# Kernel tuning notes

Hardware: AMD Instinct MI355X
Metric: run time of the kernel (lower is better)

The kernel has to match this reference:

```python
import jax, jax.numpy as jnp
import numpy as np

N_CENTROIDS = 1024
NSAMPLES = 32
RADIUS = 0.5
BN_EPS = 1e-5


def fps(xyz, npoint):
    """Iterative farthest point sampling. xyz: [B,N,3] -> idx [B,npoint] int32."""
    B, N, _ = xyz.shape

    def step(carry, _):
        dist_min, farthest = carry  # [B,N], [B]
        centroid = jnp.take_along_axis(xyz, farthest[:, None, None], axis=1)  # [B,1,3]
        d = jnp.sum((xyz - centroid) ** 2, axis=-1)  # [B,N]
        dist_min = jnp.minimum(dist_min, d)
        nxt = jnp.argmax(dist_min, axis=1).astype(jnp.int32)
        return (dist_min, nxt), farthest

    init = (jnp.full((B, N), 1e10, xyz.dtype), jnp.zeros((B,), jnp.int32))
    _, idx = jax.lax.scan(step, init, None, length=npoint)
    return idx.T  # [B, npoint]


def gather_points(p, idx):
    """p: [B,N,C], idx: [B,...] int -> [B,...,C]."""
    return jax.vmap(lambda pp, ii: pp[ii])(p, idx)


def square_distance(a, b):
    """a: [B,S,3], b: [B,N,3] -> [B,S,N] squared distances (GEMM form)."""
    aa = jnp.sum(a * a, axis=-1)[:, :, None]
    bb = jnp.sum(b * b, axis=-1)[:, None, :]
    ab = jnp.einsum('bsc,bnc->bsn', a, b)
    return aa + bb - 2.0 * ab


def ball_query(centroids, xyz, nsample, radius):
    B, S, _ = centroids.shape
    N = xyz.shape[1]
    sqrdists = square_distance(centroids, xyz)  # [B,S,N]
    base = jnp.broadcast_to(jnp.arange(N, dtype=jnp.int32), (B, S, N))
    group_idx = jnp.where(sqrdists > radius * radius, N, base)
    group_idx = jnp.sort(group_idx, axis=-1)[:, :, :nsample]  # [B,S,K]
    first = group_idx[:, :, :1]
    group_idx = jnp.where(group_idx == N, first, group_idx)
    return group_idx


def batchnorm2d(h, gamma, beta):
    """Training-mode BN over (B,H,W) per channel. h: [B,C,H,W]."""
    mean = jnp.mean(h, axis=(0, 2, 3), keepdims=True)
    var = jnp.mean((h - mean) ** 2, axis=(0, 2, 3), keepdims=True)
    hhat = (h - mean) * jax.lax.rsqrt(var + BN_EPS)
    return gamma[None, :, None, None] * hhat + beta[None, :, None, None]


def conv1x1(h, w, b):
    """h: [B,C,H,W], w: [O,C] -> [B,O,H,W]."""
    return jnp.einsum('bchw,oc->bohw', h, w) + b[None, :, None, None]


def setup_inputs() -> dict:
    key = jax.random.key(0)
    ks = jax.random.split(key, 4)
    B, N, D = 16, 4096, 3
    mlp0, mlp1, in_ch = 64, 128, 6
    return {
        'x': jax.random.normal(ks[0], (B, N, 3), jnp.float32),
        'points': jax.random.normal(ks[1], (B, N, D), jnp.float32),
        'w1': jax.random.normal(ks[2], (mlp0, in_ch), jnp.float32) * 0.1,
        'b1': jnp.zeros((mlp0,), jnp.float32),
        'gamma1': jnp.ones((mlp0,), jnp.float32),
        'beta1': jnp.zeros((mlp0,), jnp.float32),
        'w2': jax.random.normal(ks[3], (mlp1, mlp0), jnp.float32) * 0.1,
        'b2': jnp.zeros((mlp1,), jnp.float32),
        'gamma2': jnp.ones((mlp1,), jnp.float32),
        'beta2': jnp.zeros((mlp1,), jnp.float32),
    }


def reference(x, points, w1, b1, gamma1, beta1, w2, b2, gamma2, beta2):
    # FPS -> centroids
    cidx = fps(x, N_CENTROIDS)                      # [B,S]
    centroids = gather_points(x, cidx)              # [B,S,3]
    # Ball-query grouping
    idx = ball_query(centroids, x, NSAMPLES, RADIUS)  # [B,S,K]
    grouped_xyz = gather_points(x, idx) - centroids[:, :, None, :]  # [B,S,K,3]
    grouped_pts = jnp.concatenate([grouped_xyz, gather_points(points, idx)], axis=-1)  # [B,S,K,C]
    # g_points.transpose(1,3): [B,S,K,C] -> [B,C,K,S]
    h = jnp.transpose(grouped_pts, (0, 3, 2, 1))
    h = jax.nn.relu(batchnorm2d(conv1x1(h, w1, b1), gamma1, beta1))
    h = jax.nn.relu(batchnorm2d(conv1x1(h, w2, b2), gamma2, beta2))
    out = jnp.max(h, axis=2)            # [B,mlp1,S]
    out = jnp.transpose(out, (0, 2, 1))  # [B,S,mlp1]
    return centroids, out
```

## Files before the change

kernel.cpp:

```cpp
#include <hip/hip_runtime.h>
#include <stdint.h>
#include <math.h>

constexpr int BB = 16;
constexpr int NN = 4096;
constexpr int SS = 1024;
constexpr int KK = 32;
constexpr int C3 = 128;
constexpr float R2 = 0.25f;
constexpr int STAT_BLOCKS = 2048;

__device__ __forceinline__ float sumsq3(float x, float y, float z) {
#pragma clang fp contract(off)
  return (x * x + y * y) + z * z;
}

__device__ __forceinline__ float ball_d(float aa, float bb, float cx, float cy,
                                        float cz, float px, float py, float pz) {
#pragma clang fp contract(off)
  float ab = (cx * px + cy * py) + cz * pz;
  return (aa + bb) - 2.0f * ab;
}

__device__ __forceinline__ unsigned long long u64max(unsigned long long a,
                                                     unsigned long long b) {
  return a > b ? a : b;
}

#define DPP_KEY_STEP(CTRL, k)                                                  \
  {                                                                            \
    int lo_ = (int)(unsigned)(k);                                              \
    int hi_ = (int)(unsigned)((k) >> 32);                                      \
    int slo_ = __builtin_amdgcn_update_dpp(0, lo_, (CTRL), 0xf, 0xf, true);    \
    int shi_ = __builtin_amdgcn_update_dpp(0, hi_, (CTRL), 0xf, 0xf, true);    \
    unsigned long long o_ =                                                    \
        ((unsigned long long)(unsigned)shi_ << 32) | (unsigned)(unsigned)slo_; \
    (k) = u64max((k), o_);                                                     \
  }

__global__ void k_bb(const float* __restrict__ x, float* __restrict__ bb) {
  int i = blockIdx.x * blockDim.x + threadIdx.x;
  if (i >= BB * NN) return;
  float x0 = x[3 * i], x1 = x[3 * i + 1], x2 = x[3 * i + 2];
  bb[i] = sumsq3(x0, x1, x2);
}

__global__ __launch_bounds__(256) void k_fps(const float* __restrict__ x,
                                             int* __restrict__ cidx) {
  __shared__ float xs[NN], ys[NN], zs[NN];
  __shared__ unsigned long long wkey[2][4];
  int b = blockIdx.x, t = threadIdx.x;
  const float* xb = x + (size_t)b * NN * 3;
  float px[16], py[16], pz[16], dmin[16];
  unsigned lo_[16];
#pragma unroll
  for (int j = 0; j < 16; ++j) {
    int n = t + j * 256;
    float a0 = xb[3 * n], a1 = xb[3 * n + 1], a2 = xb[3 * n + 2];
    px[j] = a0; py[j] = a1; pz[j] = a2;
    xs[n] = a0; ys[n] = a1; zs[n] = a2;
    dmin[j] = 1e10f;
    lo_[j] = (unsigned)(NN - 1 - n);
  }
  if (t == 0) cidx[b * SS] = 0;
  __syncthreads();
  int far = 0;
  int w = t >> 6;
  for (int it = 1; it < SS; ++it) {
    float cx = xs[far], cy = ys[far], cz = zs[far];
    float best = -1.0f;
    unsigned blo = 0u;
#pragma unroll
    for (int j = 0; j < 16; ++j) {
      float dx = px[j] - cx, dy = py[j] - cy, dz = pz[j] - cz;
      float d = sumsq3(dx, dy, dz);
      float dm = fminf(dmin[j], d);
      dmin[j] = dm;
      if (dm > best) { best = dm; blo = lo_[j]; }
    }
    unsigned long long key =
        ((unsigned long long)__float_as_uint(best) << 32) | blo;
    DPP_KEY_STEP(0xB1, key);
    DPP_KEY_STEP(0x4E, key);
    DPP_KEY_STEP(0x124, key);
    DPP_KEY_STEP(0x128, key);
    {
      int lo2 = __builtin_amdgcn_ds_swizzle((int)(unsigned)key, 0x401F);
      int hi2 = __builtin_amdgcn_ds_swizzle((int)(unsigned)(key >> 32), 0x401F);
      unsigned long long o =
          ((unsigned long long)(unsigned)hi2 << 32) | (unsigned)lo2;
      key = u64max(key, o);
    }
    key = u64max(key, __shfl_xor(key, 32));
    int buf = it & 1;
    if ((t & 63) == 0) wkey[buf][w] = key;
    __syncthreads();
    unsigned long long k0 = wkey[buf][0], k1 = wkey[buf][1];
    unsigned long long k2 = wkey[buf][2], k3 = wkey[buf][3];
    unsigned long long kk = u64max(u64max(k0, k1), u64max(k2, k3));
    far = NN - 1 - (int)(unsigned)(kk & 0xffffffffu);
    if (t == 0) cidx[b * SS + it] = far;
  }
}

__global__ void k_gather(const float* __restrict__ x, const int* __restrict__ cidx,
                         float* __restrict__ outc, float* __restrict__ aa) {
  int i = blockIdx.x * blockDim.x + threadIdx.x;
  if (i >= BB * SS) return;
  int b = i >> 10;
  int n = cidx[i];
  const float* p = x + ((size_t)b * NN + n) * 3;
  float cx = p[0], cy = p[1], cz = p[2];
  outc[3 * i] = cx; outc[3 * i + 1] = cy; outc[3 * i + 2] = cz;
  aa[i] = sumsq3(cx, cy, cz);
}

__global__ __launch_bounds__(256) void k_ball(const float* __restrict__ x,
                                              const float* __restrict__ cent,
                                              const float* __restrict__ aa,
                                              const float* __restrict__ bb,
                                              int* __restrict__ idx) {
  int gw = (blockIdx.x * 256 + threadIdx.x) >> 6;
  int lane = threadIdx.x & 63;
  if (gw >= BB * SS) return;
  int b = gw >> 10;
  const float* xb = x + (size_t)b * NN * 3;
  const float* bbb = bb + b * NN;
  float cx = cent[3 * gw], cy = cent[3 * gw + 1], cz = cent[3 * gw + 2];
  float a = aa[gw];
  int* out = idx + (size_t)gw * KK;
  int found = 0, firstN = 0;
  for (int c0 = 0; c0 < NN && found < KK; c0 += 64) {
    int n = c0 + lane;
    float px = xb[3 * n], py = xb[3 * n + 1], pz = xb[3 * n + 2];
    float d = ball_d(a, bbb[n], cx, cy, cz, px, py, pz);
    bool pred = (d <= R2);
    unsigned long long m = __ballot(pred);
    if (found == 0 && m) firstN = c0 + (__ffsll((unsigned long long)m) - 1);
    if (pred) {
      int pos = found + __popcll(m & ((1ull << lane) - 1ull));
      if (pos < KK) out[pos] = n;
    }
    found += __popcll(m);
  }
  if (lane == 0 && found < KK) {
    for (int k = found; k < KK; ++k) out[k] = firstN;
  }
}

__global__ __launch_bounds__(256) void k_stats1(
    const float* __restrict__ x, const float* __restrict__ pts,
    const float* __restrict__ cent, const int* __restrict__ idx,
    const float* __restrict__ w1, const float* __restrict__ b1,
    float* __restrict__ partial1) {
  __shared__ float feat[KK][6];
  __shared__ float red[4][64][2];
  int t = threadIdx.x;
  int c = t & 63, kq = t >> 6;
  float w[6];
#pragma unroll
  for (int j = 0; j < 6; ++j) w[j] = w1[c * 6 + j];
  float bias = b1[c];
  float sum = 0.f, sq = 0.f;
  for (int gi = 0; gi < 8; ++gi) {
    int g = blockIdx.x * 8 + gi;
    int b = g >> 10;
    if (t < KK) {
      int n = idx[(size_t)g * KK + t];
      const float* p = x + ((size_t)b * NN + n) * 3;
      feat[t][0] = p[0] - cent[3 * g];
      feat[t][1] = p[1] - cent[3 * g + 1];
      feat[t][2] = p[2] - cent[3 * g + 2];
      const float* q = pts + ((size_t)b * NN + n) * 3;
      feat[t][3] = q[0];
      feat[t][4] = q[1];
      feat[t][5] = q[2];
    }
    __syncthreads();
    for (int k = kq * 8; k < kq * 8 + 8; ++k) {
      float a = bias;
#pragma unroll
      for (int j = 0; j < 6; ++j) a += w[j] * feat[k][j];
      sum += a;
      sq += a * a;
    }
    __syncthreads();
  }
  red[kq][c][0] = sum;
  red[kq][c][1] = sq;
  __syncthreads();
  if (t < 64) {
    float s = ((red[0][t][0] + red[1][t][0]) + red[2][t][0]) + red[3][t][0];
    float q = ((red[0][t][1] + red[1][t][1]) + red[2][t][1]) + red[3][t][1];
    partial1[(size_t)(blockIdx.x * 64 + t) * 2] = s;
    partial1[(size_t)(blockIdx.x * 64 + t) * 2 + 1] = q;
  }
}

__global__ void k_red1(const float* __restrict__ partial1,
                       const float* __restrict__ gamma, const float* __restrict__ beta,
                       float* __restrict__ sc1) {
  __shared__ double rd[64][4][2];
  int t = threadIdx.x;
  int c = t & 63, q = t >> 6;
  double s = 0.0, qq = 0.0;
  for (int blk = q * 512; blk < q * 512 + 512; ++blk) {
    s += partial1[(size_t)(blk * 64 + c) * 2];
    qq += partial1[(size_t)(blk * 64 + c) * 2 + 1];
  }
  rd[c][q][0] = s; rd[c][q][1] = qq;
  __syncthreads();
  if (t < 64) {
    double S = ((rd[t][0][0] + rd[t][1][0]) + rd[t][2][0]) + rd[t][3][0];
    double Q = ((rd[t][0][1] + rd[t][1][1]) + rd[t][2][1]) + rd[t][3][1];
    const double cnt = (double)BB * KK * SS;
    double mean = S / cnt;
    double var = Q / cnt - mean * mean;
    float scale = gamma[t] * (float)(1.0 / sqrt(var + 1e-5));
    float shift = beta[t] - (float)mean * scale;
    sc1[t] = scale;
    sc1[64 + t] = shift;
  }
}

__global__ __launch_bounds__(256) void k_stats2(
    const float* __restrict__ x, const float* __restrict__ pts,
    const float* __restrict__ cent, const int* __restrict__ idx,
    const float* __restrict__ w1, const float* __restrict__ b1,
    const float* __restrict__ sc1, const float* __restrict__ w2,
    const float* __restrict__ b2, float* __restrict__ partial2,
    float* __restrict__ gmax, float* __restrict__ gmin) {
  __shared__ float feat[KK][6];
  __shared__ float vT[64][36];
  __shared__ float w2sA[64][68];
  __shared__ float w2sB[64][68];
  __shared__ float red[C3][4][2];
  __shared__ float mx[C3][4], mn[C3][4];
  int t = threadIdx.x;
  int c1 = t & 63, kq = t >> 6;
  int c2p = t >> 2, ks = t & 3;
  {
    int r = t >> 1, h = (t & 1) * 32;
    float* dst = (r < 64 ? &w2sA[r][h] : &w2sB[r - 64][h]);
    const float* src = w2 + r * 64 + h;
    for (int c = 0; c < 32; ++c) dst[c] = src[c];
  }
  float w1r[6];
#pragma unroll
  for (int j = 0; j < 6; ++j) w1r[j] = w1[c1 * 6 + j];
  float bias1 = b1[c1];
  float scale1 = sc1[c1], shift1 = sc1[64 + c1];
  float bias2a = b2[c2p], bias2b = b2[c2p + 64];
  float sumA = 0.f, sqA = 0.f, sumB = 0.f, sqB = 0.f;
  for (int gi = 0; gi < 8; ++gi) {
    int g = blockIdx.x * 8 + gi;
    int b = g >> 10;
    if (t < KK) {
      int n = idx[(size_t)g * KK + t];
      const float* p = x + ((size_t)b * NN + n) * 3;
      feat[t][0] = p[0] - cent[3 * g];
      feat[t][1] = p[1] - cent[3 * g + 1];
      feat[t][2] = p[2] - cent[3 * g + 2];
      const float* q = pts + ((size_t)b * NN + n) * 3;
      feat[t][3] = q[0];
      feat[t][4] = q[1];
      feat[t][5] = q[2];
    }
    __syncthreads();
    for (int k = kq * 8; k < kq * 8 + 8; ++k) {
      float a = bias1;
#pragma unroll
      for (int j = 0; j < 6; ++j) a += w1r[j] * feat[k][j];
      vT[c1][k] = fmaxf(0.f, a * scale1 + shift1);
    }
    __syncthreads();
    float accA[8] = {0, 0, 0, 0, 0, 0, 0, 0};
    float accB[8] = {0, 0, 0, 0, 0, 0, 0, 0};
#pragma unroll
    for (int c0 = 0; c0 < 64; c0 += 4) {
      float4 wa4 = *(const float4*)&w2sA[c2p][c0];
      float4 wb4 = *(const float4*)&w2sB[c2p][c0];
#pragma unroll
      for (int cc = 0; cc < 4; ++cc) {
        int c = c0 + cc;
        float4 v0 = *(const float4*)&vT[c][ks * 8];
        float4 v1 = *(const float4*)&vT[c][ks * 8 + 4];
        float wa = (cc == 0 ? wa4.x : cc == 1 ? wa4.y : cc == 2 ? wa4.z : wa4.w);
        float wb = (cc == 0 ? wb4.x : cc == 1 ? wb4.y : cc == 2 ? wb4.z : wb4.w);
        accA[0] += wa * v0.x; accA[1] += wa * v0.y; accA[2] += wa * v0.z; accA[3] += wa * v0.w;
        accA[4] += wa * v1.x; accA[5] += wa * v1.y; accA[6] += wa * v1.z; accA[7] += wa * v1.w;
        accB[0] += wb * v0.x; accB[1] += wb * v0.y; accB[2] += wb * v0.z; accB[3] += wb * v0.w;
        accB[4] += wb * v1.x; accB[5] += wb * v1.y; accB[6] += wb * v1.z; accB[7] += wb * v1.w;
      }
    }
    float mA = -1e30f, mB = -1e30f, nA = 1e30f, nB = 1e30f;
#pragma unroll
    for (int i = 0; i < 8; ++i) {
      float a = accA[i] + bias2a;
      sumA += a; sqA += a * a;
      mA = fmaxf(mA, a); nA = fminf(nA, a);
      float c_ = accB[i] + bias2b;
      sumB += c_; sqB += c_ * c_;
      mB = fmaxf(mB, c_); nB = fminf(nB, c_);
    }
    mx[c2p][ks] = mA;      mn[c2p][ks] = nA;
    mx[c2p + 64][ks] = mB; mn[c2p + 64][ks] = nB;
    __syncthreads();
    if (t < C3) {
      float M = fmaxf(fmaxf(mx[t][0], mx[t][1]), fmaxf(mx[t][2], mx[t][3]));
      float m_ = fminf(fminf(mn[t][0], mn[t][1]), fminf(mn[t][2], mn[t][3]));
      gmax[(size_t)g * C3 + t] = M;
      gmin[(size_t)g * C3 + t] = m_;
    }
  }
  red[c2p][ks][0] = sumA;      red[c2p][ks][1] = sqA;
  red[c2p + 64][ks][0] = sumB; red[c2p + 64][ks][1] = sqB;
  __syncthreads();
  if (t < C3) {
    float s = ((red[t][0][0] + red[t][1][0]) + red[t][2][0]) + red[t][3][0];
    float q = ((red[t][0][1] + red[t][1][1]) + red[t][2][1]) + red[t][3][1];
    partial2[(size_t)(blockIdx.x * 128 + t) * 2] = s;
    partial2[(size_t)(blockIdx.x * 128 + t) * 2 + 1] = q;
  }
}

__global__ void k_red2(const float* __restrict__ partial2,
                       const float* __restrict__ gamma, const float* __restrict__ beta,
                       float* __restrict__ sc2) {
  __shared__ double rd[128][4][2];
  int t = threadIdx.x;
  int c = t & 127, q = t >> 7;
  double s = 0.0, qq = 0.0;
  for (int blk = q * 512; blk < q * 512 + 512; ++blk) {
    s += partial2[(size_t)(blk * 128 + c) * 2];
    qq += partial2[(size_t)(blk * 128 + c) * 2 + 1];
  }
  rd[c][q][0] = s; rd[c][q][1] = qq;
  __syncthreads();
  if (t < 128) {
    double S = ((rd[t][0][0] + rd[t][1][0]) + rd[t][2][0]) + rd[t][3][0];
    double Q = ((rd[t][0][1] + rd[t][1][1]) + rd[t][2][1]) + rd[t][3][1];
    const double cnt = (double)BB * KK * SS;
    double mean = S / cnt;
    double var = Q / cnt - mean * mean;
    float scale = gamma[t] * (float)(1.0 / sqrt(var + 1e-5));
    float shift = beta[t] - (float)mean * scale;
    sc2[t] = scale;
    sc2[128 + t] = shift;
  }
}

__global__ void k_final2(const float* __restrict__ gmin,
                         const float* __restrict__ sc2, float* __restrict__ outp) {
  int i = blockIdx.x * blockDim.x + threadIdx.x;
  if (i >= BB * SS * C3) return;
  int c = i & (C3 - 1);
  float scale = sc2[c], shift = sc2[C3 + c];
  float a = (scale >= 0.f) ? outp[i] : gmin[i];
  outp[i] = fmaxf(0.f, a * scale + shift);
}

extern "C" void kernel_launch(void* const* d_in, const int* in_sizes, int n_in,
                              void* d_out, int out_size, void* d_ws, size_t ws_size,
                              hipStream_t stream) {
  const float* x      = (const float*)d_in[0];
  const float* pts    = (const float*)d_in[1];
  const float* w1     = (const float*)d_in[2];
  const float* b1     = (const float*)d_in[3];
  const float* gamma1 = (const float*)d_in[4];
  const float* beta1  = (const float*)d_in[5];
  const float* w2     = (const float*)d_in[6];
  const float* b2     = (const float*)d_in[7];
  const float* gamma2 = (const float*)d_in[8];
  const float* beta2  = (const float*)d_in[9];

  float* out_cent = (float*)d_out;
  float* out_feat = (float*)d_out + (size_t)BB * SS * 3;

  char* w = (char*)d_ws;
  int* cidx    = (int*)w;   w += (size_t)BB * SS * 4;
  float* aa    = (float*)w; w += (size_t)BB * SS * 4;
  float* bb    = (float*)w; w += (size_t)BB * NN * 4;
  int* idx     = (int*)w;   w += (size_t)BB * SS * KK * 4;
  float* p1    = (float*)w; w += (size_t)STAT_BLOCKS * 64 * 2 * 4;
  float* p2    = (float*)w; w += (size_t)STAT_BLOCKS * 128 * 2 * 4;
  float* sc1   = (float*)w; w += 64 * 2 * 4;
  float* sc2   = (float*)w; w += 128 * 2 * 4;
  float* gmin  = (float*)w; w += (size_t)BB * SS * C3 * 4;

  k_bb<<<(BB * NN + 255) / 256, 256, 0, stream>>>(x, bb);
  k_fps<<<BB, 256, 0, stream>>>(x, cidx);
  k_gather<<<(BB * SS + 255) / 256, 256, 0, stream>>>(x, cidx, out_cent, aa);
  k_ball<<<(BB * SS) / 4, 256, 0, stream>>>(x, out_cent, aa, bb, idx);
  k_stats1<<<STAT_BLOCKS, 256, 0, stream>>>(x, pts, out_cent, idx, w1, b1, p1);
  k_red1<<<1, 256, 0, stream>>>(p1, gamma1, beta1, sc1);
  k_stats2<<<STAT_BLOCKS, 256, 0, stream>>>(x, pts, out_cent, idx, w1, b1, sc1,
                                            w2, b2, p2, out_feat, gmin);
  k_red2<<<1, 512, 0, stream>>>(p2, gamma2, beta2, sc2);
  k_final2<<<(BB * SS * C3 + 255) / 256, 256, 0, stream>>>(gmin, sc2, out_feat);
}
```

Measured before the change: 964.1 us.

## Streamline FPS reduction with float max, ballot, and broadcast centroid coordinates

```diff
diff --git a/kernel.cpp b/kernel.cpp
--- a/kernel.cpp
+++ b/kernel.cpp
@@ -27,16 +27,23 @@
   return a > b ? a : b;
 }
 
-#define DPP_KEY_STEP(CTRL, k)                                                  \
+#define DPP_MAXF(CTRL, v)                                                      \
   {                                                                            \
-    int lo_ = (int)(unsigned)(k);                                              \
-    int hi_ = (int)(unsigned)((k) >> 32);                                      \
-    int slo_ = __builtin_amdgcn_update_dpp(0, lo_, (CTRL), 0xf, 0xf, true);    \
-    int shi_ = __builtin_amdgcn_update_dpp(0, hi_, (CTRL), 0xf, 0xf, true);    \
-    unsigned long long o_ =                                                    \
-        ((unsigned long long)(unsigned)shi_ << 32) | (unsigned)(unsigned)slo_; \
-    (k) = u64max((k), o_);                                                     \
-  }
+    int s_ = __builtin_amdgcn_update_dpp(0, __float_as_int(v), (CTRL), 0xf,    \
+                                         0xf, true);                           \
+    (v) = fmaxf((v), __int_as_float(s_));                                      \
+  }
+
+__device__ __forceinline__ float xor32maxf(float v) {
+#if __has_builtin(__builtin_amdgcn_permlane32_swap)
+  typedef int v2i __attribute__((ext_vector_type(2)));
+  v2i r = __builtin_amdgcn_permlane32_swap(__float_as_int(v), __float_as_int(v),
+                                           false, false);
+  return fmaxf(fmaxf(v, __int_as_float(r[0])), __int_as_float(r[1]));
+#else
+  return fmaxf(v, __shfl_xor(v, 32));
+#endif
+}
 
 __global__ void k_bb(const float* __restrict__ x, float* __restrict__ bb) {
   int i = blockIdx.x * blockDim.x + threadIdx.x;
@@ -47,60 +54,68 @@
 
 __global__ __launch_bounds__(256) void k_fps(const float* __restrict__ x,
                                              int* __restrict__ cidx) {
-  __shared__ float xs[NN], ys[NN], zs[NN];
   __shared__ unsigned long long wkey[2][4];
+  __shared__ float4 wxyz[2][4];
+  __shared__ int farhist[SS];
   int b = blockIdx.x, t = threadIdx.x;
   const float* xb = x + (size_t)b * NN * 3;
   float px[16], py[16], pz[16], dmin[16];
-  unsigned lo_[16];
-#pragma unroll
-  for (int j = 0; j < 16; ++j) {
-    int n = t + j * 256;
-    float a0 = xb[3 * n], a1 = xb[3 * n + 1], a2 = xb[3 * n + 2];
-    px[j] = a0; py[j] = a1; pz[j] = a2;
-    xs[n] = a0; ys[n] = a1; zs[n] = a2;
-    dmin[j] = 1e10f;
-    lo_[j] = (unsigned)(NN - 1 - n);
-  }
-  if (t == 0) cidx[b * SS] = 0;
-  __syncthreads();
-  int far = 0;
-  int w = t >> 6;
+  {
+    float4 f[12];
+    const float4* src = (const float4*)(xb + t * 48);
+#pragma unroll
+    for (int i = 0; i < 12; ++i) f[i] = src[i];
+    const float* s = (const float*)f;
+#pragma unroll
+    for (int j = 0; j < 16; ++j) {
+      px[j] = s[3 * j]; py[j] = s[3 * j + 1]; pz[j] = s[3 * j + 2];
+      dmin[j] = 1e10f;
+    }
+  }
+  float cx = xb[0], cy = xb[1], cz = xb[2];
+  if (t == 0) farhist[0] = 0;
+  int w = t >> 6, lane = t & 63;
+  __syncthreads();
   for (int it = 1; it < SS; ++it) {
-    float cx = xs[far], cy = ys[far], cz = zs[far];
     float best = -1.0f;
-    unsigned blo = 0u;
+    int bj = 0;
 #pragma unroll
     for (int j = 0; j < 16; ++j) {
       float dx = px[j] - cx, dy = py[j] - cy, dz = pz[j] - cz;
       float d = sumsq3(dx, dy, dz);
       float dm = fminf(dmin[j], d);
       dmin[j] = dm;
-      if (dm > best) { best = dm; blo = lo_[j]; }
-    }
-    unsigned long long key =
-        ((unsigned long long)__float_as_uint(best) << 32) | blo;
-    DPP_KEY_STEP(0xB1, key);
-    DPP_KEY_STEP(0x4E, key);
-    DPP_KEY_STEP(0x124, key);
-    DPP_KEY_STEP(0x128, key);
-    {
-      int lo2 = __builtin_amdgcn_ds_swizzle((int)(unsigned)key, 0x401F);
-      int hi2 = __builtin_amdgcn_ds_swizzle((int)(unsigned)(key >> 32), 0x401F);
-      unsigned long long o =
-          ((unsigned long long)(unsigned)hi2 << 32) | (unsigned)lo2;
-      key = u64max(key, o);
-    }
-    key = u64max(key, __shfl_xor(key, 32));
+      if (dm > best) { best = dm; bj = j; }
+    }
+    float wmax = best;
+    DPP_MAXF(0xB1, wmax);
+    DPP_MAXF(0x4E, wmax);
+    DPP_MAXF(0x124, wmax);
+    DPP_MAXF(0x128, wmax);
+    wmax = fmaxf(wmax, __int_as_float(__builtin_amdgcn_ds_swizzle(
+                     __float_as_int(wmax), 0x401F)));
+    wmax = xor32maxf(wmax);
+    unsigned long long mb = __ballot(best == wmax);
+    int wl = __ffsll(mb) - 1;
     int buf = it & 1;
-    if ((t & 63) == 0) wkey[buf][w] = key;
+    if (lane == wl) {
+      int n = t * 16 + bj;
+      wkey[buf][w] =
+          ((unsigned long long)__float_as_uint(wmax) << 32) | (unsigned)(NN - 1 - n);
+      wxyz[buf][w] = make_float4(px[bj], py[bj], pz[bj], 0.f);
+    }
     __syncthreads();
     unsigned long long k0 = wkey[buf][0], k1 = wkey[buf][1];
     unsigned long long k2 = wkey[buf][2], k3 = wkey[buf][3];
+    float4 r0 = wxyz[buf][0], r1 = wxyz[buf][1];
+    float4 r2 = wxyz[buf][2], r3 = wxyz[buf][3];
     unsigned long long kk = u64max(u64max(k0, k1), u64max(k2, k3));
-    far = NN - 1 - (int)(unsigned)(kk & 0xffffffffu);
-    if (t == 0) cidx[b * SS + it] = far;
-  }
+    float4 cc = (kk == k0) ? r0 : (kk == k1) ? r1 : (kk == k2) ? r2 : r3;
+    cx = cc.x; cy = cc.y; cz = cc.z;
+    if (t == 0) farhist[it] = NN - 1 - (int)(unsigned)(kk & 0xffffffffu);
+  }
+  __syncthreads();
+  for (int i = t; i < SS; i += 256) cidx[b * SS + i] = farhist[i];
 }
 
 __global__ void k_gather(const float* __restrict__ x, const int* __restrict__ cidx,
```

After: 1.395 ms. 44.7% more time.
